# Performance work log

Hardware: AMD Instinct MI355X
Metric: run time of the kernel (lower is better)

Reference implementation:

```python
import jax, jax.numpy as jnp
import numpy as np

# Model dims (match init_kwargs)
B, H, W, C = 16, 6, 4096, 128
OVERLAP, NUM_PVQS, NUM_RVQS = 4, 3, 6
CB_DIM, CB_SIZE = 8, 1024
FIX = H * C                          # fix_dim = in_freq*in_dim = 768
HIDDEN = FIX * OVERLAP // NUM_PVQS   # 1024 per product group


def setup_inputs() -> dict:
    key = jax.random.key(0)
    k1, k2, k3, k4 = jax.random.split(key, 4)
    return {
        "z_e": jax.random.normal(k1, (B, H * W, C), jnp.float32),
        # per-(product-group, residual-stage) codebooks
        "embeds": jax.random.normal(k2, (NUM_PVQS, NUM_RVQS, CB_SIZE, CB_DIM), jnp.float32),
        # nn.Linear(hidden, codebook_dim, bias=False) stored as (hidden, cb_dim) so y = x @ W
        "proj_down": jax.random.normal(k3, (NUM_PVQS, HIDDEN, CB_DIM), jnp.float32) * (HIDDEN ** -0.5),
        "proj_up": jax.random.normal(k4, (NUM_PVQS, CB_DIM, HIDDEN), jnp.float32) * (CB_DIM ** -0.5),
        "num_streams": 6,
    }


def _l2n(x, eps=1e-12):
    return x / jnp.maximum(jnp.linalg.norm(x, axis=-1, keepdims=True), eps)


def _codebook(residual, embed):
    """One VQ codebook (l2norm variant): cdist + argmin + lookup + ST estimator.
    residual: (B, T, d); embed: (K, d)."""
    z = _l2n(residual)
    e = _l2n(embed)
    # squared euclidean distances (B, T, K)
    d = (z * z).sum(-1, keepdims=True) - 2.0 * jnp.einsum('btd,kd->btk', z, e) + (e * e).sum(-1)
    code = jnp.argmin(d, axis=-1)                      # (B, T) int
    q = jnp.take(e, code, axis=0)                      # (B, T, d)
    cb_loss = jnp.mean((q - jax.lax.stop_gradient(residual)) ** 2)
    cm_loss = jnp.mean((residual - jax.lax.stop_gradient(q)) ** 2)
    z_q = residual + jax.lax.stop_gradient(q - residual)   # straight-through
    return z_q, code, cb_loss, cm_loss


def reference(z_e, embeds, proj_down, proj_up, num_streams):
    # pre_process (dims=3): 'b (h w) c -> b w (c h)' then fold overlap frames
    x = z_e.reshape(B, H, W, C).transpose(0, 2, 3, 1).reshape(B, W, FIX)
    T = W // OVERLAP
    x = x.reshape(B, T, OVERLAP * FIX)

    zq_parts, code_parts = [], []
    cb_loss = 0.0
    cm_loss = 0.0
    for m in range(NUM_PVQS):
        xm = x[..., m * HIDDEN:(m + 1) * HIDDEN]
        residual = xm @ proj_down[m]                   # (B, T, CB_DIM)
        zq_m = jnp.zeros_like(residual)
        codes_m = []
        for i in range(num_streams):                   # residual VQ stages
            qi, ci, cb, cm = _codebook(residual, embeds[m, i])
            residual = residual - qi
            zq_m = zq_m + qi
            codes_m.append(ci)
            cb_loss = cb_loss + cb
            cm_loss = cm_loss + cm
        zq_parts.append(zq_m @ proj_up[m])             # (B, T, HIDDEN)
        code_parts.append(jnp.stack(codes_m, axis=1))  # (B, num_streams, T)

    zq = jnp.concatenate(zq_parts, axis=-1)            # (B, T, OVERLAP*FIX)
    codes = jnp.stack(code_parts, axis=2)              # (B, num_streams, num_pvqs, T)

    # post_process (dims=3): unfold overlap, 'b w (c h) -> b (h w) c'
    zq = zq.reshape(B, W, FIX).reshape(B, W, C, H).transpose(0, 3, 1, 2).reshape(B, H * W, C)
    return zq, codes, cb_loss / NUM_PVQS, cm_loss / NUM_PVQS
```

## Files before the change

### kernel.cpp

```cpp
#include <hip/hip_runtime.h>

#define BB        16
#define HH        6
#define WW        4096
#define CC        128
#define TT        1024
#define NTOK      16384
#define FIX       768
#define HID       1024
#define CBK       1024
#define CBD       8
#define NPVQ      3
#define NRVQ      6
#define ZQ_SIZE   50331648ull

#define OFF_ACC   0ull
#define OFF_EN64  16ull
#define OFF_EN32  (OFF_EN64 + 1179648ull)
#define OFF_PUT   (OFF_EN32 + 589824ull)
#define OFF_R     (OFF_PUT + 98304ull)
#define OFF_ZQ    (OFF_R + 3145728ull)

__global__ __launch_bounds__(256) void knorm(const float* __restrict__ emb,
                                             double* __restrict__ en64,
                                             float* __restrict__ en32) {
    int gid = blockIdx.x * 256 + threadIdx.x;
    if (gid >= NPVQ * NRVQ * CBK) return;
    const float* e = emb + (size_t)gid * CBD;
    double v[CBD];
    double s = 0.0;
#pragma unroll
    for (int d = 0; d < CBD; ++d) { v[d] = (double)e[d]; s += v[d] * v[d]; }
    double n = fmax(sqrt(s), 1e-12);
#pragma unroll
    for (int d = 0; d < CBD; ++d) {
        double q = v[d] / n;
        en64[(size_t)gid * CBD + d] = q;
        en32[(size_t)gid * CBD + d] = (float)q;
    }
}

__global__ __launch_bounds__(256) void kputr(const float* __restrict__ pu,
                                             float* __restrict__ pu_t) {
    int gid = blockIdx.x * 256 + threadIdx.x;
    if (gid >= NPVQ * CBD * HID) return;
    int j = gid & (HID - 1), md = gid >> 10;
    int m = md >> 3, d = md & 7;
    pu_t[((size_t)m * HID + j) * CBD + d] = pu[gid];
}

__global__ __launch_bounds__(384) void kproj(const float* __restrict__ ze,
                                             const float* __restrict__ pd,
                                             double* __restrict__ r_ws) {
    __shared__ float x[2][NPVQ * HID];
    const int tok0 = blockIdx.x * 2;
    const int b = tok0 >> 10, t0 = tok0 & 1023;
    const int tid = threadIdx.x;
    const size_t zbase = (size_t)b * (HH * WW * CC);
#pragma unroll
    for (int q = 0; q < 4; ++q) {
        int g = tid + 384 * q;
        int tk = g >= 768;
        int gg = g - tk * 768;
        int h = gg >> 7, v = gg & 127;
        const float4 val = *(const float4*)(ze + zbase + (size_t)(h * WW + (t0 + tk) * 4) * CC + v * 4);
        float vv[4] = {val.x, val.y, val.z, val.w};
#pragma unroll
        for (int e = 0; e < 4; ++e) {
            int oc = v * 4 + e, o = oc >> 7, c = oc & 127;
            x[tk][o * FIX + c * HH + h] = vv[e];
        }
    }
    __syncthreads();
    const int w = tid >> 6, l = tid & 63;
    const int tk = w >= 3, m = w - tk * 3;
    double acc[CBD] = {0, 0, 0, 0, 0, 0, 0, 0};
    for (int q = 0; q < 16; ++q) {
        int j = l + 64 * q;
        double xv = (double)x[tk][m * HID + j];
        const float* pr = pd + (size_t)(m * HID + j) * CBD;
#pragma unroll
        for (int d = 0; d < CBD; ++d) acc[d] = fma(xv, (double)pr[d], acc[d]);
    }
#pragma unroll
    for (int off = 32; off >= 1; off >>= 1) {
#pragma unroll
        for (int d = 0; d < CBD; ++d) acc[d] += __shfl_down(acc[d], off, 64);
    }
    if (l == 0) {
        double* rp = r_ws + ((size_t)m * NTOK + tok0 + tk) * CBD;
#pragma unroll
        for (int d = 0; d < CBD; ++d) rp[d] = acc[d];
    }
}

#define KV_WAVES    8
#define KV_THREADS  (KV_WAVES * 64)
#define KV_WSLICE   (CBK / KV_WAVES)
#define KV_EPS      2e-6f
#define KV_EPS_CAND 2e-6f

__global__ __launch_bounds__(KV_THREADS) void kvq(const double* __restrict__ en_all,
                                                  const float* __restrict__ es_all,
                                                  const double* __restrict__ r_ws,
                                                  float* __restrict__ zq_ws,
                                                  float* __restrict__ out,
                                                  const int* __restrict__ nsp,
                                                  double* __restrict__ accum) {
    __shared__ __align__(16) float tbl[CBK * CBD];
    __shared__ float  mb1[KV_THREADS];
    __shared__ float  mb2[KV_THREADS];
    __shared__ int    mbk[KV_THREADS];
    __shared__ double md64[KV_THREADS];
    __shared__ int    mk64[KV_THREADS];

    const int blk = blockIdx.x;
    const int m = blk >> 8, g = blk & 255;
    const int tid = threadIdx.x;
    const int w = tid >> 6, l = tid & 63;
    const int tok = g * 64 + l;
    const int b = tok >> 10, t = tok & 1023;
    const int ns = *nsp;

    double r[CBD];
    {
        const double* rp = r_ws + ((size_t)m * NTOK + tok) * CBD;
#pragma unroll
        for (int d = 0; d < CBD; ++d) r[d] = rp[d];
    }
    double zq[CBD] = {0, 0, 0, 0, 0, 0, 0, 0};
    double loss = 0.0;

    const int kl0 = w * KV_WSLICE;
    for (int i = 0; i < ns; ++i) {
        const double* en = en_all + ((size_t)(m * NRVQ + i)) * CBK * CBD;
        const float*  es = es_all + ((size_t)(m * NRVQ + i)) * CBK * CBD;
        double s = 0.0;
#pragma unroll
        for (int d = 0; d < CBD; ++d) s += r[d] * r[d];
        double inv = 1.0 / fmax(sqrt(s), 1e-12);
        float rn[CBD];
#pragma unroll
        for (int d = 0; d < CBD; ++d) rn[d] = (float)(r[d] * inv);

        __syncthreads();
        {
            const float4* src = (const float4*)es;
            float4* dst = (float4*)tbl;
#pragma unroll
            for (int q = 0; q < 4; ++q) dst[tid + KV_THREADS * q] = src[tid + KV_THREADS * q];
        }
        __syncthreads();

        float b1 = -1e30f, b2 = -1e30f;
        int bk = kl0;
        for (int k = kl0; k < kl0 + KV_WSLICE; k += 4) {
            float dots[4];
#pragma unroll
            for (int u = 0; u < 4; ++u) {
                const float* ev = tbl + (size_t)(k + u) * CBD;
                float a0 = 0.0f, a1 = 0.0f;
#pragma unroll
                for (int d = 0; d < CBD; d += 2) {
                    a0 = fmaf(rn[d], ev[d], a0);
                    a1 = fmaf(rn[d + 1], ev[d + 1], a1);
                }
                dots[u] = a0 + a1;
            }
#pragma unroll
            for (int u = 0; u < 4; ++u) {
                float dv = dots[u];
                if (dv > b1) { b2 = b1; b1 = dv; bk = k + u; }
                else if (dv > b2) { b2 = dv; }
            }
        }
        mb1[tid] = b1; mb2[tid] = b2; mbk[tid] = bk;
        __syncthreads();
        float B1 = mb1[l], B2 = mb2[l];
        int K = mbk[l];
#pragma unroll
        for (int w2 = 1; w2 < KV_WAVES; ++w2) {
            float c1 = mb1[w2 * 64 + l];
            float c2 = mb2[w2 * 64 + l];
            int   ck = mbk[w2 * 64 + l];
            if (c1 > B1) { B2 = fmaxf(B1, c2); B1 = c1; K = ck; }
            else         { B2 = fmaxf(B2, c1); }
        }
        int bbk = K;
        bool uncert = (B1 - B2) <= KV_EPS;
        if (__any(uncert)) {
            __syncthreads();
            double rb = -1e300;
            int rk = CBK;
            for (int k = kl0; k < kl0 + KV_WSLICE; ++k) {
                const float* ev = tbl + (size_t)k * CBD;
                float a0 = 0.0f, a1 = 0.0f;
#pragma unroll
                for (int d = 0; d < CBD; d += 2) {
                    a0 = fmaf(rn[d], ev[d], a0);
                    a1 = fmaf(rn[d + 1], ev[d + 1], a1);
                }
                float dv = a0 + a1;
                if (uncert && dv >= B1 - KV_EPS_CAND) {
                    const double* e64 = en + (size_t)k * CBD;
                    double q0 = 0.0, q1 = 0.0;
#pragma unroll
                    for (int d = 0; d < CBD; d += 2) {
                        q0 = fma(r[d], e64[d], q0);
                        q1 = fma(r[d + 1], e64[d + 1], q1);
                    }
                    double dot = q0 + q1;
                    if (dot > rb || (dot == rb && k < rk)) { rb = dot; rk = k; }
                }
            }
            md64[tid] = rb; mk64[tid] = rk;
            __syncthreads();
            if (uncert) {
                double R = md64[l];
                int RK = mk64[l];
#pragma unroll
                for (int w2 = 1; w2 < KV_WAVES; ++w2) {
                    double d2 = md64[w2 * 64 + l];
                    int    k2 = mk64[w2 * 64 + l];
                    if (d2 > R || (d2 == R && k2 < RK)) { R = d2; RK = k2; }
                }
                bbk = RK;
            }
        }
        const double* qv = en + (size_t)bbk * CBD;
        if (w == 0) {
            double ls = 0.0;
#pragma unroll
            for (int d = 0; d < CBD; ++d) { double df = qv[d] - r[d]; ls += df * df; }
            loss += ls;
            out[ZQ_SIZE + ((size_t)(b * ns + i) * NPVQ + m) * TT + t] = (float)bbk;
        }
#pragma unroll
        for (int d = 0; d < CBD; ++d) { double q = qv[d]; r[d] -= q; zq[d] += q; }
    }

    if (w == 0) {
        float* zp = zq_ws + ((size_t)m * NTOK + tok) * CBD;
#pragma unroll
        for (int d = 0; d < CBD; ++d) zp[d] = (float)zq[d];
#pragma unroll
        for (int off = 32; off >= 1; off >>= 1) loss += __shfl_down(loss, off, 64);
        if (l == 0) atomicAdd(accum, loss);
    }
}

__global__ __launch_bounds__(256) void kout(const float* __restrict__ pu_t,
                                            const float* __restrict__ zq_ws,
                                            float* __restrict__ out,
                                            const int* __restrict__ nsp,
                                            const double* __restrict__ accum) {
    __shared__ float zl[32][NPVQ][CBD];
    const int blk = blockIdx.x;
    const int tok0 = blk * 32;
    const int b = tok0 >> 10, t0 = tok0 & 1023;
    const int tid = threadIdx.x;
#pragma unroll
    for (int q = 0; q < 3; ++q) {
        int ii = tid + 256 * q;
        int mm = ii >> 8, rem = ii & 255, tt = rem >> 3, d = rem & 7;
        zl[tt][mm][d] = zq_ws[((size_t)mm * NTOK + tok0 + tt) * CBD + d];
    }
    __syncthreads();
    const size_t obase = (size_t)b * (HH * WW * CC);
#pragma unroll 2
    for (int q = 0; q < 12; ++q) {
        int idx = tid + 256 * q;
        int h = idx >> 9, rem = idx & 511, o = rem >> 7, c = rem & 127;
        int f = o * FIX + c * HH + h;
        int m = f >> 10, j = f & 1023;
        const float4* p4 = (const float4*)(pu_t + ((size_t)m * HID + j) * CBD);
        float4 pa = p4[0], pb = p4[1];
        float pu8[CBD] = {pa.x, pa.y, pa.z, pa.w, pb.x, pb.y, pb.z, pb.w};
        size_t rowbase = obase + ((size_t)h * WW + t0 * 4 + o) * CC + c;
        for (int tt = 0; tt < 32; ++tt) {
            float y = 0.0f;
#pragma unroll
            for (int d = 0; d < CBD; ++d) y = fmaf(zl[tt][m][d], pu8[d], y);
            out[rowbase + (size_t)tt * 4 * CC] = y;
        }
    }
    if (blk == 0 && tid == 0) {
        int ns = *nsp;
        double s = *accum;
        float lv = (float)(s / (double)(NTOK * CBD * NPVQ));
        size_t lbase = ZQ_SIZE + (size_t)BB * ns * NPVQ * TT;
        out[lbase] = lv;
        out[lbase + 1] = lv;
    }
}

extern "C" void kernel_launch(void* const* d_in, const int* in_sizes, int n_in,
                              void* d_out, int out_size, void* d_ws, size_t ws_size,
                              hipStream_t stream) {
    const float* ze  = (const float*)d_in[0];
    const float* emb = (const float*)d_in[1];
    const float* pd  = (const float*)d_in[2];
    const float* pu  = (const float*)d_in[3];
    const int*   nsp = (const int*)d_in[4];
    float* out = (float*)d_out;
    char* ws = (char*)d_ws;

    double* accum = (double*)(ws + OFF_ACC);
    double* en64  = (double*)(ws + OFF_EN64);
    float*  en32  = (float*)(ws + OFF_EN32);
    float*  pu_t  = (float*)(ws + OFF_PUT);
    double* r_ws  = (double*)(ws + OFF_R);
    float*  zq_ws = (float*)(ws + OFF_ZQ);

    hipMemsetAsync(accum, 0, 16, stream);
    knorm<<<(NPVQ * NRVQ * CBK + 255) / 256, 256, 0, stream>>>(emb, en64, en32);
    kputr<<<(NPVQ * CBD * HID + 255) / 256, 256, 0, stream>>>(pu, pu_t);
    kproj<<<NTOK / 2, 384, 0, stream>>>(ze, pd, r_ws);
    kvq<<<NPVQ * (NTOK / 64), KV_THREADS, 0, stream>>>(en64, en32, r_ws, zq_ws, out, nsp, accum);
    kout<<<NTOK / 32, 256, 0, stream>>>(pu_t, zq_ws, out, nsp, accum);
}
```

Measured before the change: 330.0 us.

## Read codebook via uniform scalar loads, merge prep kernels, pack FMAs in output

The VQ kernel no longer stages each codebook into LDS. Each wave reads its 128-entry codebook slice directly from global memory with a wave-uniform base (readfirstlane), so the loads can become scalar/broadcast loads. This removes the LDS copy and two barriers per stage. The fp64 refinement pass now loads codebook entries only when some lane in the wave is a candidate, and the zq accumulator becomes fp32. The two small prep kernels are merged into one launch, launch bounds ask for two blocks per CU, and the output projection uses float4 LDS reads with packed 2-wide FMAs. The risks are more global/scalar-cache traffic in place of LDS reads, and slight fp32 rounding differences in zq.

```diff
diff --git a/kernel.cpp b/kernel.cpp
--- a/kernel.cpp
+++ b/kernel.cpp
@@ -21,32 +21,36 @@
 #define OFF_R     (OFF_PUT + 98304ull)
 #define OFF_ZQ    (OFF_R + 3145728ull)
 
-__global__ __launch_bounds__(256) void knorm(const float* __restrict__ emb,
+typedef float v2f __attribute__((ext_vector_type(2)));
+
+__global__ __launch_bounds__(256) void kprep(const float* __restrict__ emb,
                                              double* __restrict__ en64,
-                                             float* __restrict__ en32) {
-    int gid = blockIdx.x * 256 + threadIdx.x;
-    if (gid >= NPVQ * NRVQ * CBK) return;
-    const float* e = emb + (size_t)gid * CBD;
-    double v[CBD];
-    double s = 0.0;
-#pragma unroll
-    for (int d = 0; d < CBD; ++d) { v[d] = (double)e[d]; s += v[d] * v[d]; }
-    double n = fmax(sqrt(s), 1e-12);
-#pragma unroll
-    for (int d = 0; d < CBD; ++d) {
-        double q = v[d] / n;
-        en64[(size_t)gid * CBD + d] = q;
-        en32[(size_t)gid * CBD + d] = (float)q;
-    }
-}
-
-__global__ __launch_bounds__(256) void kputr(const float* __restrict__ pu,
+                                             float* __restrict__ en32,
+                                             const float* __restrict__ pu,
                                              float* __restrict__ pu_t) {
-    int gid = blockIdx.x * 256 + threadIdx.x;
-    if (gid >= NPVQ * CBD * HID) return;
-    int j = gid & (HID - 1), md = gid >> 10;
-    int m = md >> 3, d = md & 7;
-    pu_t[((size_t)m * HID + j) * CBD + d] = pu[gid];
+    const int bid = blockIdx.x;
+    if (bid < 72) {
+        int gid = bid * 256 + threadIdx.x;
+        if (gid >= NPVQ * NRVQ * CBK) return;
+        const float* e = emb + (size_t)gid * CBD;
+        double v[CBD];
+        double s = 0.0;
+#pragma unroll
+        for (int d = 0; d < CBD; ++d) { v[d] = (double)e[d]; s += v[d] * v[d]; }
+        double n = fmax(sqrt(s), 1e-12);
+#pragma unroll
+        for (int d = 0; d < CBD; ++d) {
+            double q = v[d] / n;
+            en64[(size_t)gid * CBD + d] = q;
+            en32[(size_t)gid * CBD + d] = (float)q;
+        }
+    } else {
+        int gid = (bid - 72) * 256 + threadIdx.x;
+        if (gid >= NPVQ * CBD * HID) return;
+        int j = gid & (HID - 1), md = gid >> 10;
+        int m = md >> 3, d = md & 7;
+        pu_t[((size_t)m * HID + j) * CBD + d] = pu[gid];
+    }
 }
 
 __global__ __launch_bounds__(384) void kproj(const float* __restrict__ ze,
@@ -97,17 +101,17 @@
 #define KV_WAVES    8
 #define KV_THREADS  (KV_WAVES * 64)
 #define KV_WSLICE   (CBK / KV_WAVES)
+#define KV_TILE     4
 #define KV_EPS      2e-6f
 #define KV_EPS_CAND 2e-6f
 
-__global__ __launch_bounds__(KV_THREADS) void kvq(const double* __restrict__ en_all,
-                                                  const float* __restrict__ es_all,
-                                                  const double* __restrict__ r_ws,
-                                                  float* __restrict__ zq_ws,
-                                                  float* __restrict__ out,
-                                                  const int* __restrict__ nsp,
-                                                  double* __restrict__ accum) {
-    __shared__ __align__(16) float tbl[CBK * CBD];
+__global__ __launch_bounds__(KV_THREADS, 2) void kvq(const double* __restrict__ en_all,
+                                                     const float* __restrict__ es_all,
+                                                     const double* __restrict__ r_ws,
+                                                     float* __restrict__ zq_ws,
+                                                     float* __restrict__ out,
+                                                     const int* __restrict__ nsp,
+                                                     double* __restrict__ accum) {
     __shared__ float  mb1[KV_THREADS];
     __shared__ float  mb2[KV_THREADS];
     __shared__ int    mbk[KV_THREADS];
@@ -128,10 +132,13 @@
 #pragma unroll
         for (int d = 0; d < CBD; ++d) r[d] = rp[d];
     }
-    double zq[CBD] = {0, 0, 0, 0, 0, 0, 0, 0};
+    float zq[CBD];
+#pragma unroll
+    for (int d = 0; d < CBD; ++d) zq[d] = 0.0f;
     double loss = 0.0;
 
-    const int kl0 = w * KV_WSLICE;
+    const int k0s = __builtin_amdgcn_readfirstlane(w * KV_WSLICE);
+
     for (int i = 0; i < ns; ++i) {
         const double* en = en_all + ((size_t)(m * NRVQ + i)) * CBK * CBD;
         const float*  es = es_all + ((size_t)(m * NRVQ + i)) * CBK * CBD;
@@ -143,37 +150,30 @@
 #pragma unroll
         for (int d = 0; d < CBD; ++d) rn[d] = (float)(r[d] * inv);
 
-        __syncthreads();
-        {
-            const float4* src = (const float4*)es;
-            float4* dst = (float4*)tbl;
-#pragma unroll
-            for (int q = 0; q < 4; ++q) dst[tid + KV_THREADS * q] = src[tid + KV_THREADS * q];
-        }
-        __syncthreads();
-
         float b1 = -1e30f, b2 = -1e30f;
-        int bk = kl0;
-        for (int k = kl0; k < kl0 + KV_WSLICE; k += 4) {
-            float dots[4];
-#pragma unroll
-            for (int u = 0; u < 4; ++u) {
-                const float* ev = tbl + (size_t)(k + u) * CBD;
+        int bk = k0s;
+        for (int kt = 0; kt < KV_WSLICE; kt += KV_TILE) {
+            const int kb = k0s + kt;
+            float ek[KV_TILE][CBD];
+#pragma unroll
+            for (int c = 0; c < KV_TILE; ++c)
+#pragma unroll
+                for (int d = 0; d < CBD; ++d)
+                    ek[c][d] = es[(size_t)(kb + c) * CBD + d];
+#pragma unroll
+            for (int c = 0; c < KV_TILE; ++c) {
                 float a0 = 0.0f, a1 = 0.0f;
 #pragma unroll
                 for (int d = 0; d < CBD; d += 2) {
-                    a0 = fmaf(rn[d], ev[d], a0);
-                    a1 = fmaf(rn[d + 1], ev[d + 1], a1);
+                    a0 = fmaf(rn[d], ek[c][d], a0);
+                    a1 = fmaf(rn[d + 1], ek[c][d + 1], a1);
                 }
-                dots[u] = a0 + a1;
-            }
-#pragma unroll
-            for (int u = 0; u < 4; ++u) {
-                float dv = dots[u];
-                if (dv > b1) { b2 = b1; b1 = dv; bk = k + u; }
+                float dv = a0 + a1;
+                if (dv > b1) { b2 = b1; b1 = dv; bk = kb + c; }
                 else if (dv > b2) { b2 = dv; }
             }
         }
+        __syncthreads();
         mb1[tid] = b1; mb2[tid] = b2; mbk[tid] = bk;
         __syncthreads();
         float B1 = mb1[l], B2 = mb2[l];
@@ -192,25 +192,39 @@
             __syncthreads();
             double rb = -1e300;
             int rk = CBK;
-            for (int k = kl0; k < kl0 + KV_WSLICE; ++k) {
-                const float* ev = tbl + (size_t)k * CBD;
-                float a0 = 0.0f, a1 = 0.0f;
-#pragma unroll
-                for (int d = 0; d < CBD; d += 2) {
-                    a0 = fmaf(rn[d], ev[d], a0);
-                    a1 = fmaf(rn[d + 1], ev[d + 1], a1);
-                }
-                float dv = a0 + a1;
-                if (uncert && dv >= B1 - KV_EPS_CAND) {
-                    const double* e64 = en + (size_t)k * CBD;
-                    double q0 = 0.0, q1 = 0.0;
+            for (int kt = 0; kt < KV_WSLICE; kt += KV_TILE) {
+                const int kb = k0s + kt;
+                float ek[KV_TILE][CBD];
+#pragma unroll
+                for (int c = 0; c < KV_TILE; ++c)
+#pragma unroll
+                    for (int d = 0; d < CBD; ++d)
+                        ek[c][d] = es[(size_t)(kb + c) * CBD + d];
+#pragma unroll
+                for (int c = 0; c < KV_TILE; ++c) {
+                    float a0 = 0.0f, a1 = 0.0f;
 #pragma unroll
                     for (int d = 0; d < CBD; d += 2) {
-                        q0 = fma(r[d], e64[d], q0);
-                        q1 = fma(r[d + 1], e64[d + 1], q1);
+                        a0 = fmaf(rn[d], ek[c][d], a0);
+                        a1 = fmaf(rn[d + 1], ek[c][d + 1], a1);
                     }
-                    double dot = q0 + q1;
-                    if (dot > rb || (dot == rb && k < rk)) { rb = dot; rk = k; }
+                    float dv = a0 + a1;
+                    bool cand = uncert && (dv >= B1 - KV_EPS_CAND);
+                    if (__any(cand)) {
+                        double e64[CBD];
+#pragma unroll
+                        for (int d = 0; d < CBD; ++d) e64[d] = en[(size_t)(kb + c) * CBD + d];
+                        double q0 = 0.0, q1 = 0.0;
+#pragma unroll
+                        for (int d = 0; d < CBD; d += 2) {
+                            q0 = fma(r[d], e64[d], q0);
+                            q1 = fma(r[d + 1], e64[d + 1], q1);
+                        }
+                        double dot = q0 + q1;
+                        if (cand && (dot > rb || (dot == rb && (kb + c) < rk))) {
+                            rb = dot; rk = kb + c;
+                        }
+                    }
                 }
             }
             md64[tid] = rb; mk64[tid] = rk;
@@ -236,13 +250,17 @@
             out[ZQ_SIZE + ((size_t)(b * ns + i) * NPVQ + m) * TT + t] = (float)bbk;
         }
 #pragma unroll
-        for (int d = 0; d < CBD; ++d) { double q = qv[d]; r[d] -= q; zq[d] += q; }
+        for (int d = 0; d < CBD; ++d) {
+            double q = qv[d];
+            r[d] -= q;
+            zq[d] += (float)q;
+        }
     }
 
     if (w == 0) {
         float* zp = zq_ws + ((size_t)m * NTOK + tok) * CBD;
 #pragma unroll
-        for (int d = 0; d < CBD; ++d) zp[d] = (float)zq[d];
+        for (int d = 0; d < CBD; ++d) zp[d] = zq[d];
 #pragma unroll
         for (int off = 32; off >= 1; off >>= 1) loss += __shfl_down(loss, off, 64);
         if (l == 0) atomicAdd(accum, loss);
@@ -275,13 +293,22 @@
         int m = f >> 10, j = f & 1023;
         const float4* p4 = (const float4*)(pu_t + ((size_t)m * HID + j) * CBD);
         float4 pa = p4[0], pb = p4[1];
-        float pu8[CBD] = {pa.x, pa.y, pa.z, pa.w, pb.x, pb.y, pb.z, pb.w};
+        v2f pw[4];
+        pw[0].x = pa.x; pw[0].y = pa.y;
+        pw[1].x = pa.z; pw[1].y = pa.w;
+        pw[2].x = pb.x; pw[2].y = pb.y;
+        pw[3].x = pb.z; pw[3].y = pb.w;
         size_t rowbase = obase + ((size_t)h * WW + t0 * 4 + o) * CC + c;
         for (int tt = 0; tt < 32; ++tt) {
-            float y = 0.0f;
-#pragma unroll
-            for (int d = 0; d < CBD; ++d) y = fmaf(zl[tt][m][d], pu8[d], y);
-            out[rowbase + (size_t)tt * 4 * CC] = y;
+            const float4* z4 = (const float4*)&zl[tt][m][0];
+            float4 za = z4[0], zb = z4[1];
+            v2f acc = {0.0f, 0.0f};
+            v2f zz;
+            zz.x = za.x; zz.y = za.y; acc = __builtin_elementwise_fma(zz, pw[0], acc);
+            zz.x = za.z; zz.y = za.w; acc = __builtin_elementwise_fma(zz, pw[1], acc);
+            zz.x = zb.x; zz.y = zb.y; acc = __builtin_elementwise_fma(zz, pw[2], acc);
+            zz.x = zb.z; zz.y = zb.w; acc = __builtin_elementwise_fma(zz, pw[3], acc);
+            out[rowbase + (size_t)tt * 4 * CC] = acc.x + acc.y;
         }
     }
     if (blk == 0 && tid == 0) {
@@ -313,8 +340,7 @@
     float*  zq_ws = (float*)(ws + OFF_ZQ);
 
     hipMemsetAsync(accum, 0, 16, stream);
-    knorm<<<(NPVQ * NRVQ * CBK + 255) / 256, 256, 0, stream>>>(emb, en64, en32);
-    kputr<<<(NPVQ * CBD * HID + 255) / 256, 256, 0, stream>>>(pu, pu_t);
+    kprep<<<168, 256, 0, stream>>>(emb, en64, en32, pu, pu_t);
     kproj<<<NTOK / 2, 384, 0, stream>>>(ze, pd, r_ws);
     kvq<<<NPVQ * (NTOK / 64), KV_THREADS, 0, stream>>>(en64, en32, r_ws, zq_ws, out, nsp, accum);
     kout<<<NTOK / 32, 256, 0, stream>>>(pu_t, zq_ws, out, nsp, accum);
```

Result: slower. 377.6 us (+14.4%).
